# Performance work log

Hardware: AMD Instinct MI355X
Metric: run time of the kernel (lower is better)

## Reference

```python
import jax, jax.numpy as jnp
import numpy as np
from jax import lax

SCORE_TH = 0.05
IOU_TH = 0.5
MAX_DET = 100  # fixed keep budget per class (torch version is variable-length; we pad)
BBOX_STD = jnp.array([0.1, 0.1, 0.2, 0.2], dtype=jnp.float32)


def setup_inputs() -> dict:
    key = jax.random.key(0)
    k1, k2, k3, k4 = jax.random.split(key, 4)
    A, C, H, W = 200000, 80, 768, 768
    # sigmoid-like scores, skewed low so the 0.05 threshold is meaningful
    classification = jax.random.uniform(k1, (A, C), dtype=jnp.float32) ** 4
    regression = jax.random.normal(k2, (A, 4), dtype=jnp.float32)
    ctr = jax.random.uniform(k3, (A, 2), dtype=jnp.float32, minval=0.0, maxval=float(W))
    wh = jax.random.uniform(k4, (A, 2), dtype=jnp.float32, minval=8.0, maxval=128.0)
    anchors = jnp.concatenate([ctr - 0.5 * wh, ctr + 0.5 * wh], axis=-1)  # valid x1y1x2y2
    return {"classification": classification, "regression": regression,
            "anchors": anchors, "img_h": H, "img_w": W}


def _decode_clip(anchors, regression, img_h, img_w):
    # BBoxTransform: RetinaNet delta decode with std [0.1,0.1,0.2,0.2], then ClipBoxes
    wa = anchors[:, 2] - anchors[:, 0]
    ha = anchors[:, 3] - anchors[:, 1]
    cxa = anchors[:, 0] + 0.5 * wa
    cya = anchors[:, 1] + 0.5 * ha
    d = regression * BBOX_STD
    cx = cxa + d[:, 0] * wa
    cy = cya + d[:, 1] * ha
    w = jnp.exp(d[:, 2]) * wa
    h = jnp.exp(d[:, 3]) * ha
    boxes = jnp.stack([cx - 0.5 * w, cy - 0.5 * h, cx + 0.5 * w, cy + 0.5 * h], axis=-1)
    lim = jnp.array([img_w, img_h, img_w, img_h], dtype=boxes.dtype)
    return jnp.clip(boxes, 0.0, lim)


def _nms_one(scores_c, boxes, areas):
    # greedy NMS for one class over all A anchors; fixed MAX_DET iterations
    s0 = jnp.where(scores_c > SCORE_TH, scores_c, -1.0)

    def step(s, _):
        i = jnp.argmax(s)
        valid = s[i] > 0.0
        b = boxes[i]
        xx1 = jnp.maximum(b[0], boxes[:, 0])
        yy1 = jnp.maximum(b[1], boxes[:, 1])
        xx2 = jnp.minimum(b[2], boxes[:, 2])
        yy2 = jnp.minimum(b[3], boxes[:, 3])
        inter = jnp.maximum(xx2 - xx1, 0.0) * jnp.maximum(yy2 - yy1, 0.0)
        iou = inter / (areas[i] + areas - inter)
        supp = (iou > IOU_TH) & valid
        s = jnp.where(supp, -1.0, s).at[i].set(-1.0)
        return s, (i, valid)

    _, (idx, val) = lax.scan(step, s0, None, length=MAX_DET)
    return idx, val  # [MAX_DET] int, [MAX_DET] bool


def _forward(classification, regression, anchors, img_h, img_w):
    boxes = _decode_clip(anchors, regression, img_h, img_w)  # [A,4]
    # NMS index selection is non-differentiable (as in torch); stop_gradient the selection path
    boxes_ng = lax.stop_gradient(boxes)
    scores_ng = lax.stop_gradient(classification)
    areas = (boxes_ng[:, 2] - boxes_ng[:, 0]) * (boxes_ng[:, 3] - boxes_ng[:, 1])
    idx, val = jax.vmap(_nms_one, in_axes=(1, None, None))(scores_ng, boxes_ng, areas)  # [C,M]
    C = classification.shape[1]
    sel_scores = jnp.take_along_axis(classification.T, idx, axis=1) * val          # [C,M]
    sel_boxes = boxes[idx] * val[..., None]                                        # [C,M,4]
    class_ids = jnp.where(val, jnp.arange(C, dtype=jnp.int32)[:, None], -1)        # [C,M]
    # torch returns variable-length concatenations; we return fixed-size padded
    # equivalents (invalid slots: score=0, class=-1, box=0)
    return sel_scores.reshape(-1), class_ids.reshape(-1), sel_boxes.reshape(-1, 4)


def reference(classification, regression, anchors, img_h, img_w):
    return _forward(classification, regression, anchors, img_h, img_w)
```

## Files before the change

### kernel.cpp

```cpp
#include <hip/hip_runtime.h>
#include <float.h>
#include <math.h>

#define SCORE_TH 0.05f
#define IOU_TH   0.5f
#define MAXD     100
#define CAP      512
#define HI_TH    0.996f
#define SWALK    192
#define NWORDS   3
#define CNT_STRIDE 16

__device__ __forceinline__ float4 decode_box(float4 an, float4 r, float W, float H)
{
    float wa = an.z - an.x, ha = an.w - an.y;
    float cxa = an.x + 0.5f * wa, cya = an.y + 0.5f * ha;
    float cx = cxa + r.x * 0.1f * wa;
    float cy = cya + r.y * 0.1f * ha;
    float w  = expf(r.z * 0.2f) * wa;
    float h  = expf(r.w * 0.2f) * ha;
    float x1 = cx - 0.5f * w, y1 = cy - 0.5f * h;
    float x2 = cx + 0.5f * w, y2 = cy + 0.5f * h;
    x1 = fminf(fmaxf(x1, 0.f), W);
    y1 = fminf(fmaxf(y1, 0.f), H);
    x2 = fminf(fmaxf(x2, 0.f), W);
    y2 = fminf(fmaxf(y2, 0.f), H);
    return make_float4(x1, y1, x2, y2);
}

template<int CC>
__global__ __launch_bounds__(256)
void k_compact(const float4* __restrict__ cls4, float2* __restrict__ cand,
               int* __restrict__ cnt, int* __restrict__ loflag,
               int C_rt, int total4)
{
    const int C = CC ? CC : C_rt;
    __shared__ unsigned char lflag[256];
    for (int i = threadIdx.x; i < C; i += blockDim.x) lflag[i] = 0;
    __syncthreads();

    const int gstride = gridDim.x * blockDim.x;
    const int gtid = blockIdx.x * blockDim.x + threadIdx.x;

    for (int j0 = gtid; j0 < total4; j0 += 4 * gstride) {
        int j1 = j0 + gstride, j2 = j0 + 2 * gstride, j3 = j0 + 3 * gstride;
        bool ok1 = j1 < total4, ok2 = j2 < total4, ok3 = j3 < total4;
        float4 v0 = cls4[j0];
        float4 v1 = ok1 ? cls4[j1] : make_float4(0.f, 0.f, 0.f, 0.f);
        float4 v2 = ok2 ? cls4[j2] : make_float4(0.f, 0.f, 0.f, 0.f);
        float4 v3 = ok3 ? cls4[j3] : make_float4(0.f, 0.f, 0.f, 0.f);

        #pragma unroll
        for (int w = 0; w < 4; w++) {
            float4 v = (w == 0) ? v0 : (w == 1) ? v1 : (w == 2) ? v2 : v3;
            if (w == 1 && !ok1) break;
            if (w == 2 && !ok2) break;
            if (w == 3 && !ok3) break;
            unsigned b = (unsigned)(j0 + w * gstride) * 4u;
            int c = (int)(b % (unsigned)C);
            int a = (int)(b / (unsigned)C);
            float s[4] = {v.x, v.y, v.z, v.w};
            #pragma unroll
            for (int j = 0; j < 4; j++) {
                float sc = s[j];
                if (sc > HI_TH) {
                    int pos = atomicAdd(&cnt[c * CNT_STRIDE], 1);
                    if (pos < CAP) cand[(size_t)c * CAP + pos] = make_float2(sc, __int_as_float(a));
                } else if (sc > SCORE_TH) {
                    lflag[c] = 1;
                }
                c++; if (c == C) { c = 0; a++; }
            }
        }
    }
    __syncthreads();
    for (int i = threadIdx.x; i < C; i += blockDim.x)
        if (lflag[i]) loflag[i] = 1;
}

__device__ void fallback_class(const float* __restrict__ cls,
                               const float4* __restrict__ anch, const float4* __restrict__ reg,
                               float W, float H, int A, int C, int c,
                               float* __restrict__ out)
{
    __shared__ float kx1[MAXD], ky1[MAXD], kx2[MAXD], ky2[MAXD], kar[MAXD];
    __shared__ float rs[4]; __shared__ int ra[4];
    __shared__ float cs; __shared__ int caid; __shared__ int have; __shared__ int suppflag;
    int lane = threadIdx.x & 63, wid = threadIdx.x >> 6;
    float s_last = FLT_MAX; int a_last = -1;
    int kept = 0;
    int total = C * MAXD;
    for (long long guard = 0; guard <= (long long)A && kept < MAXD; guard++) {
        float bs = -1.f; int ba = 0x7fffffff;
        for (int a = threadIdx.x; a < A; a += blockDim.x) {
            float s = cls[(size_t)a * C + c];
            if (s <= SCORE_TH) continue;
            if (s > s_last || (s == s_last && a <= a_last)) continue;
            if (s > bs || (s == bs && a < ba)) { bs = s; ba = a; }
        }
        for (int off = 32; off >= 1; off >>= 1) {
            float s2 = __shfl_down(bs, off);
            int a2 = __shfl_down(ba, off);
            if (s2 > bs || (s2 == bs && a2 < ba)) { bs = s2; ba = a2; }
        }
        if (lane == 0) { rs[wid] = bs; ra[wid] = ba; }
        __syncthreads();
        if (threadIdx.x == 0) {
            float fs = rs[0]; int fa = ra[0];
            for (int w = 1; w < 4; w++)
                if (rs[w] > fs || (rs[w] == fs && ra[w] < fa)) { fs = rs[w]; fa = ra[w]; }
            cs = fs; caid = fa; have = (fs > 0.f) ? 1 : 0;
        }
        __syncthreads();
        if (!have) break;
        float s_c = cs; int a_c = caid;
        s_last = s_c; a_last = a_c;
        float4 b = decode_box(anch[a_c], reg[a_c], W, H);
        float ar = (b.z - b.x) * (b.w - b.y);
        if (threadIdx.x == 0) suppflag = 0;
        __syncthreads();
        for (int k = threadIdx.x; k < kept; k += blockDim.x) {
            float xx1 = fmaxf(b.x, kx1[k]);
            float yy1 = fmaxf(b.y, ky1[k]);
            float xx2 = fminf(b.z, kx2[k]);
            float yy2 = fminf(b.w, ky2[k]);
            float inter = fmaxf(xx2 - xx1, 0.f) * fmaxf(yy2 - yy1, 0.f);
            float iou = inter / (ar + kar[k] - inter);
            if (iou > IOU_TH) suppflag = 1;
        }
        __syncthreads();
        if (!suppflag) {
            if (threadIdx.x == 0) {
                kx1[kept] = b.x; ky1[kept] = b.y; kx2[kept] = b.z; ky2[kept] = b.w; kar[kept] = ar;
                int slot = c * MAXD + kept;
                out[slot] = s_c;
                out[total + slot] = (float)c;
                float* ob = out + 2 * (size_t)total + (size_t)slot * 4;
                ob[0] = b.x; ob[1] = b.y; ob[2] = b.z; ob[3] = b.w;
            }
            kept++;
        }
        __syncthreads();
    }
    for (int k = kept + threadIdx.x; k < MAXD; k += blockDim.x) {
        int slot = c * MAXD + k;
        out[slot] = 0.f;
        out[total + slot] = -1.f;
        float* ob = out + 2 * (size_t)total + (size_t)slot * 4;
        ob[0] = 0.f; ob[1] = 0.f; ob[2] = 0.f; ob[3] = 0.f;
    }
}

__global__ __launch_bounds__(256)
void k_nms(const float* __restrict__ cls,
           const float4* __restrict__ anch, const float4* __restrict__ reg,
           const int* __restrict__ ph, const int* __restrict__ pw,
           const float2* __restrict__ cand, const int* __restrict__ cnt,
           const int* __restrict__ loflag,
           float* __restrict__ out, int A, int C)
{
    int c = blockIdx.x;
    __shared__ __align__(16) unsigned long long keys_raw[CAP];
    __shared__ unsigned long long keys[SWALK];
    __shared__ float bx1[SWALK], by1[SWALK], bx2[SWALK], by2[SWALK], sar[SWALK];
    __shared__ __align__(16) unsigned long long m0[SWALK], m1[SWALK], m2[SWALK];
    __shared__ int kidx[MAXD];

    float W = (float)(*pw), H = (float)(*ph);
    int n_raw = cnt[c * CNT_STRIDE];
    if (n_raw > CAP) {
        fallback_class(cls, anch, reg, W, H, A, C, c, out);
        return;
    }
    int n = n_raw;
    int nS = n < SWALK ? n : SWALK;

    for (int i = threadIdx.x; i < n; i += blockDim.x) {
        float2 e = cand[(size_t)c * CAP + i];
        unsigned sbits = __float_as_uint(e.x);
        unsigned aid   = (unsigned)__float_as_int(e.y);
        keys_raw[i] = ((unsigned long long)(~sbits) << 32) | (unsigned long long)aid;
    }
    __syncthreads();

    for (int i = threadIdx.x; i < n; i += blockDim.x) {
        unsigned long long ki = keys_raw[i];
        int r = 0;
        int j = 0;
        for (; j + 2 <= n; j += 2) {
            ulonglong2 kj = *(const ulonglong2*)&keys_raw[j];
            r += (kj.x < ki) + (kj.y < ki);
        }
        if (j < n) r += (keys_raw[j] < ki);
        if (r < SWALK) {
            keys[r] = ki;
            unsigned aid = (unsigned)ki;
            float4 b = decode_box(anch[aid], reg[aid], W, H);
            bx1[r] = b.x; by1[r] = b.y; bx2[r] = b.z; by2[r] = b.w;
            sar[r] = (b.z - b.x) * (b.w - b.y);
        }
    }
    __syncthreads();

    for (int task = threadIdx.x; task < nS * NWORDS; task += blockDim.x) {
        int i = task / NWORDS;
        int w = task - i * NWORDS;
        unsigned long long m = 0ull;
        int j0 = w << 6;
        int jend = j0 + 64 < nS ? j0 + 64 : nS;
        int js = j0 > i + 1 ? j0 : i + 1;
        float ix1 = bx1[i], iy1 = by1[i], ix2 = bx2[i], iy2 = by2[i], ia = sar[i];
        for (int j = js; j < jend; ++j) {
            float xx1 = fmaxf(ix1, bx1[j]);
            float yy1 = fmaxf(iy1, by1[j]);
            float xx2 = fminf(ix2, bx2[j]);
            float yy2 = fminf(iy2, by2[j]);
            float inter = fmaxf(xx2 - xx1, 0.f) * fmaxf(yy2 - yy1, 0.f);
            float iou = inter / (ia + sar[j] - inter);
            if (iou > IOU_TH) m |= 1ull << (j - j0);
        }
        if (w == 0) m0[i] = m; else if (w == 1) m1[i] = m; else m2[i] = m;
    }
    __syncthreads();

    unsigned long long rem0 = 0, rem1 = 0, rem2 = 0;
    int kept = 0;
    ulonglong2 A0 = *(const ulonglong2*)&m0[0], A1 = *(const ulonglong2*)&m0[2];
    ulonglong2 B0 = *(const ulonglong2*)&m1[0], B1 = *(const ulonglong2*)&m1[2];
    ulonglong2 Q0 = *(const ulonglong2*)&m2[0], Q1 = *(const ulonglong2*)&m2[2];
    for (int k0 = 0; k0 < nS && kept < MAXD; k0 += 4) {
        ulonglong2 nA0, nA1, nB0, nB1, nQ0, nQ1;
        int kn = k0 + 4;
        if (kn < nS) {
            nA0 = *(const ulonglong2*)&m0[kn]; nA1 = *(const ulonglong2*)&m0[kn + 2];
            nB0 = *(const ulonglong2*)&m1[kn]; nB1 = *(const ulonglong2*)&m1[kn + 2];
            nQ0 = *(const ulonglong2*)&m2[kn]; nQ1 = *(const ulonglong2*)&m2[kn + 2];
        }
        unsigned long long g = A0.x | A0.y | A1.x | A1.y | B0.x | B0.y | B1.x | B1.y
                             | Q0.x | Q0.y | Q1.x | Q1.y;
        unsigned long long rw4 = ((k0 < 64) ? rem0 : (k0 < 128) ? rem1 : rem2) >> (k0 & 63);
        if (g == 0ull && (rw4 & 0xFull) == 0ull && k0 + 4 <= nS && kept + 4 <= MAXD) {
            if (threadIdx.x == 0) {
                kidx[kept] = k0; kidx[kept + 1] = k0 + 1;
                kidx[kept + 2] = k0 + 2; kidx[kept + 3] = k0 + 3;
            }
            kept += 4;
        } else {
            #pragma unroll
            for (int s = 0; s < 4; ++s) {
                int k = k0 + s;
                if (k < nS && kept < MAXD) {
                    unsigned long long mm0 = (s == 0) ? A0.x : (s == 1) ? A0.y : (s == 2) ? A1.x : A1.y;
                    unsigned long long mm1 = (s == 0) ? B0.x : (s == 1) ? B0.y : (s == 2) ? B1.x : B1.y;
                    unsigned long long mm2 = (s == 0) ? Q0.x : (s == 1) ? Q0.y : (s == 2) ? Q1.x : Q1.y;
                    unsigned long long rw = (k < 64) ? rem0 : (k < 128) ? rem1 : rem2;
                    if (!((rw >> (k & 63)) & 1ull)) {
                        if (threadIdx.x == 0) kidx[kept] = k;
                        ++kept;
                        rem0 |= mm0; rem1 |= mm1; rem2 |= mm2;
                    }
                }
            }
        }
        A0 = nA0; A1 = nA1; B0 = nB0; B1 = nB1; Q0 = nQ0; Q1 = nQ1;
    }
    __syncthreads();

    if (kept < MAXD && (n > nS || loflag[c] != 0)) {
        fallback_class(cls, anch, reg, W, H, A, C, c, out);
        return;
    }

    int total = C * MAXD;
    int base = c * MAXD;
    for (int m = threadIdx.x; m < kept; m += blockDim.x) {
        int k = kidx[m];
        unsigned long long key = keys[k];
        float sc = __uint_as_float(~(unsigned)(key >> 32));
        out[base + m] = sc;
        out[total + base + m] = (float)c;
        float* ob = out + 2 * (size_t)total + (size_t)(base + m) * 4;
        ob[0] = bx1[k]; ob[1] = by1[k]; ob[2] = bx2[k]; ob[3] = by2[k];
    }
    for (int m = kept + threadIdx.x; m < MAXD; m += blockDim.x) {
        out[base + m] = 0.f;
        out[total + base + m] = -1.f;
        float* ob = out + 2 * (size_t)total + (size_t)(base + m) * 4;
        ob[0] = 0.f; ob[1] = 0.f; ob[2] = 0.f; ob[3] = 0.f;
    }
}

extern "C" void kernel_launch(void* const* d_in, const int* in_sizes, int n_in,
                              void* d_out, int out_size, void* d_ws, size_t ws_size,
                              hipStream_t stream)
{
    const float*  cls  = (const float*)d_in[0];
    const float4* reg  = (const float4*)d_in[1];
    const float4* anch = (const float4*)d_in[2];
    const int*    ph   = (const int*)d_in[3];
    const int*    pw   = (const int*)d_in[4];
    int A = in_sizes[1] / 4;
    int C = in_sizes[0] / A;
    float* out = (float*)d_out;

    char* ws = (char*)d_ws;
    float2* cand = (float2*)ws;
    int* ctrl   = (int*)(cand + (size_t)C * CAP);
    int* cnt    = ctrl;
    int* loflag = ctrl + C * CNT_STRIDE;

    hipMemsetAsync(ctrl, 0, (C * CNT_STRIDE + C) * sizeof(int), stream);

    int total4 = (int)((long long)A * C / 4);
    int blocks2 = (total4 + 255) / 256;
    if (blocks2 > 2048) blocks2 = 2048;
    if (C == 80 && (long long)A * C < (1LL << 31))
        k_compact<80><<<blocks2, 256, 0, stream>>>((const float4*)cls, cand, cnt, loflag, C, total4);
    else
        k_compact<0><<<blocks2, 256, 0, stream>>>((const float4*)cls, cand, cnt, loflag, C, total4);

    k_nms<<<C, 256, 0, stream>>>(cls, anch, reg, ph, pw, cand, cnt, loflag, out, A, C);
}
```

Baseline: 136.2 us.

## Decode boxes during compaction and replace serial NMS walk with parallel fixed-point iteration

Box decode and area computation move into the compaction kernel, so each candidate record carries its box and the NMS kernel skips the dependent gather from anchors and regression. The suppression matrix is transposed so each candidate holds a mask of earlier boxes that suppress it. The single-thread greedy walk becomes a block-wide fixed-point iteration: each thread tests whether any currently-kept predecessor suppresses it, and ballots form the new keep mask until it stops changing. Output positions come from popcounts. Costs are a larger candidate record, more shared memory, and an iteration count that can approach the chain length, each round paying two block barriers.

```diff
diff --git a/kernel.cpp b/kernel.cpp
--- a/kernel.cpp
+++ b/kernel.cpp
@@ -28,9 +28,14 @@
     return make_float4(x1, y1, x2, y2);
 }
 
+struct CandRec { float4 a; float4 b; };
+
 template<int CC>
 __global__ __launch_bounds__(256)
-void k_compact(const float4* __restrict__ cls4, float2* __restrict__ cand,
+void k_compact(const float4* __restrict__ cls4,
+               const float4* __restrict__ anch, const float4* __restrict__ reg,
+               const int* __restrict__ ph, const int* __restrict__ pw,
+               CandRec* __restrict__ cand,
                int* __restrict__ cnt, int* __restrict__ loflag,
                int C_rt, int total4)
 {
@@ -39,6 +44,7 @@
     for (int i = threadIdx.x; i < C; i += blockDim.x) lflag[i] = 0;
     __syncthreads();
 
+    float W = (float)(*pw), H = (float)(*ph);
     const int gstride = gridDim.x * blockDim.x;
     const int gtid = blockIdx.x * blockDim.x + threadIdx.x;
 
@@ -65,7 +71,13 @@
                 float sc = s[j];
                 if (sc > HI_TH) {
                     int pos = atomicAdd(&cnt[c * CNT_STRIDE], 1);
-                    if (pos < CAP) cand[(size_t)c * CAP + pos] = make_float2(sc, __int_as_float(a));
+                    if (pos < CAP) {
+                        float4 bx = decode_box(anch[a], reg[a], W, H);
+                        float area = (bx.z - bx.x) * (bx.w - bx.y);
+                        CandRec* r = &cand[(size_t)c * CAP + pos];
+                        r->a = make_float4(sc, __int_as_float(a), bx.x, bx.y);
+                        r->b = make_float4(bx.z, bx.w, area, 0.f);
+                    }
                 } else if (sc > SCORE_TH) {
                     lflag[c] = 1;
                 }
@@ -155,18 +167,23 @@
 void k_nms(const float* __restrict__ cls,
            const float4* __restrict__ anch, const float4* __restrict__ reg,
            const int* __restrict__ ph, const int* __restrict__ pw,
-           const float2* __restrict__ cand, const int* __restrict__ cnt,
+           const CandRec* __restrict__ cand, const int* __restrict__ cnt,
            const int* __restrict__ loflag,
            float* __restrict__ out, int A, int C)
 {
     int c = blockIdx.x;
     __shared__ __align__(16) unsigned long long keys_raw[CAP];
+    __shared__ float4 box_u[CAP];
+    __shared__ float  sar_u[CAP];
     __shared__ unsigned long long keys[SWALK];
-    __shared__ float bx1[SWALK], by1[SWALK], bx2[SWALK], by2[SWALK], sar[SWALK];
-    __shared__ __align__(16) unsigned long long m0[SWALK], m1[SWALK], m2[SWALK];
-    __shared__ int kidx[MAXD];
+    __shared__ float4 box[SWALK];
+    __shared__ float  sar[SWALK];
+    __shared__ unsigned long long t0[SWALK], t1[SWALK], t2[SWALK];
+    __shared__ unsigned long long kw[NWORDS], newkw[NWORDS];
+    __shared__ int changed;
 
     float W = (float)(*pw), H = (float)(*ph);
+    int tid = threadIdx.x;
     int n_raw = cnt[c * CNT_STRIDE];
     if (n_raw > CAP) {
         fallback_class(cls, anch, reg, W, H, A, C, c, out);
@@ -175,15 +192,17 @@
     int n = n_raw;
     int nS = n < SWALK ? n : SWALK;
 
-    for (int i = threadIdx.x; i < n; i += blockDim.x) {
-        float2 e = cand[(size_t)c * CAP + i];
-        unsigned sbits = __float_as_uint(e.x);
-        unsigned aid   = (unsigned)__float_as_int(e.y);
+    for (int i = tid; i < n; i += blockDim.x) {
+        CandRec rec = cand[(size_t)c * CAP + i];
+        unsigned sbits = __float_as_uint(rec.a.x);
+        unsigned aid   = (unsigned)__float_as_int(rec.a.y);
         keys_raw[i] = ((unsigned long long)(~sbits) << 32) | (unsigned long long)aid;
-    }
-    __syncthreads();
-
-    for (int i = threadIdx.x; i < n; i += blockDim.x) {
+        box_u[i] = make_float4(rec.a.z, rec.a.w, rec.b.x, rec.b.y);
+        sar_u[i] = rec.b.z;
+    }
+    __syncthreads();
+
+    for (int i = tid; i < n; i += blockDim.x) {
         unsigned long long ki = keys_raw[i];
         int r = 0;
         int j = 0;
@@ -194,95 +213,91 @@
         if (j < n) r += (keys_raw[j] < ki);
         if (r < SWALK) {
             keys[r] = ki;
-            unsigned aid = (unsigned)ki;
-            float4 b = decode_box(anch[aid], reg[aid], W, H);
-            bx1[r] = b.x; by1[r] = b.y; bx2[r] = b.z; by2[r] = b.w;
-            sar[r] = (b.z - b.x) * (b.w - b.y);
-        }
-    }
-    __syncthreads();
-
-    for (int task = threadIdx.x; task < nS * NWORDS; task += blockDim.x) {
-        int i = task / NWORDS;
-        int w = task - i * NWORDS;
+            box[r] = box_u[i];
+            sar[r] = sar_u[i];
+        }
+    }
+    __syncthreads();
+
+    for (int task = tid; task < nS * NWORDS; task += blockDim.x) {
+        int k = task / NWORDS;
+        int w = task - k * NWORDS;
         unsigned long long m = 0ull;
-        int j0 = w << 6;
-        int jend = j0 + 64 < nS ? j0 + 64 : nS;
-        int js = j0 > i + 1 ? j0 : i + 1;
-        float ix1 = bx1[i], iy1 = by1[i], ix2 = bx2[i], iy2 = by2[i], ia = sar[i];
-        for (int j = js; j < jend; ++j) {
-            float xx1 = fmaxf(ix1, bx1[j]);
-            float yy1 = fmaxf(iy1, by1[j]);
-            float xx2 = fminf(ix2, bx2[j]);
-            float yy2 = fminf(iy2, by2[j]);
-            float inter = fmaxf(xx2 - xx1, 0.f) * fmaxf(yy2 - yy1, 0.f);
-            float iou = inter / (ia + sar[j] - inter);
-            if (iou > IOU_TH) m |= 1ull << (j - j0);
-        }
-        if (w == 0) m0[i] = m; else if (w == 1) m1[i] = m; else m2[i] = m;
-    }
-    __syncthreads();
-
-    unsigned long long rem0 = 0, rem1 = 0, rem2 = 0;
-    int kept = 0;
-    ulonglong2 A0 = *(const ulonglong2*)&m0[0], A1 = *(const ulonglong2*)&m0[2];
-    ulonglong2 B0 = *(const ulonglong2*)&m1[0], B1 = *(const ulonglong2*)&m1[2];
-    ulonglong2 Q0 = *(const ulonglong2*)&m2[0], Q1 = *(const ulonglong2*)&m2[2];
-    for (int k0 = 0; k0 < nS && kept < MAXD; k0 += 4) {
-        ulonglong2 nA0, nA1, nB0, nB1, nQ0, nQ1;
-        int kn = k0 + 4;
-        if (kn < nS) {
-            nA0 = *(const ulonglong2*)&m0[kn]; nA1 = *(const ulonglong2*)&m0[kn + 2];
-            nB0 = *(const ulonglong2*)&m1[kn]; nB1 = *(const ulonglong2*)&m1[kn + 2];
-            nQ0 = *(const ulonglong2*)&m2[kn]; nQ1 = *(const ulonglong2*)&m2[kn + 2];
-        }
-        unsigned long long g = A0.x | A0.y | A1.x | A1.y | B0.x | B0.y | B1.x | B1.y
-                             | Q0.x | Q0.y | Q1.x | Q1.y;
-        unsigned long long rw4 = ((k0 < 64) ? rem0 : (k0 < 128) ? rem1 : rem2) >> (k0 & 63);
-        if (g == 0ull && (rw4 & 0xFull) == 0ull && k0 + 4 <= nS && kept + 4 <= MAXD) {
-            if (threadIdx.x == 0) {
-                kidx[kept] = k0; kidx[kept + 1] = k0 + 1;
-                kidx[kept + 2] = k0 + 2; kidx[kept + 3] = k0 + 3;
+        int i0 = w << 6;
+        int iend = (i0 + 64 < k) ? (i0 + 64) : k;
+        if (i0 < iend) {
+            float4 bk = box[k]; float ak = sar[k];
+            for (int i = i0; i < iend; ++i) {
+                float4 bi = box[i];
+                float xx1 = fmaxf(bk.x, bi.x);
+                float yy1 = fmaxf(bk.y, bi.y);
+                float xx2 = fminf(bk.z, bi.z);
+                float yy2 = fminf(bk.w, bi.w);
+                float inter = fmaxf(xx2 - xx1, 0.f) * fmaxf(yy2 - yy1, 0.f);
+                float iou = inter / (ak + sar[i] - inter);
+                if (iou > IOU_TH) m |= 1ull << (i - i0);
             }
-            kept += 4;
-        } else {
-            #pragma unroll
-            for (int s = 0; s < 4; ++s) {
-                int k = k0 + s;
-                if (k < nS && kept < MAXD) {
-                    unsigned long long mm0 = (s == 0) ? A0.x : (s == 1) ? A0.y : (s == 2) ? A1.x : A1.y;
-                    unsigned long long mm1 = (s == 0) ? B0.x : (s == 1) ? B0.y : (s == 2) ? B1.x : B1.y;
-                    unsigned long long mm2 = (s == 0) ? Q0.x : (s == 1) ? Q0.y : (s == 2) ? Q1.x : Q1.y;
-                    unsigned long long rw = (k < 64) ? rem0 : (k < 128) ? rem1 : rem2;
-                    if (!((rw >> (k & 63)) & 1ull)) {
-                        if (threadIdx.x == 0) kidx[kept] = k;
-                        ++kept;
-                        rem0 |= mm0; rem1 |= mm1; rem2 |= mm2;
-                    }
-                }
-            }
-        }
-        A0 = nA0; A1 = nA1; B0 = nB0; B1 = nB1; Q0 = nQ0; Q1 = nQ1;
-    }
-    __syncthreads();
-
-    if (kept < MAXD && (n > nS || loflag[c] != 0)) {
+        }
+        if (w == 0) t0[k] = m; else if (w == 1) t1[k] = m; else t2[k] = m;
+    }
+    if (tid == 0) {
+        kw[0] = (nS >= 64) ? ~0ull : ((nS <= 0) ? 0ull : ((1ull << nS) - 1));
+        int r1 = nS - 64;
+        kw[1] = (r1 >= 64) ? ~0ull : ((r1 <= 0) ? 0ull : ((1ull << r1) - 1));
+        int r2 = nS - 128;
+        kw[2] = (r2 >= 64) ? ~0ull : ((r2 <= 0) ? 0ull : ((1ull << r2) - 1));
+    }
+    __syncthreads();
+
+    for (int iter = 0; iter <= nS; ++iter) {
+        bool kept_k = false;
+        if (tid < nS) {
+            unsigned long long r = (t0[tid] & kw[0]) | (t1[tid] & kw[1]) | (t2[tid] & kw[2]);
+            kept_k = (r == 0ull);
+        }
+        unsigned long long b = __ballot(kept_k);
+        if ((tid & 63) == 0 && (tid >> 6) < NWORDS) newkw[tid >> 6] = b;
+        __syncthreads();
+        if (tid == 0) {
+            changed = (newkw[0] != kw[0]) || (newkw[1] != kw[1]) || (newkw[2] != kw[2]);
+            kw[0] = newkw[0]; kw[1] = newkw[1]; kw[2] = newkw[2];
+        }
+        __syncthreads();
+        if (!changed) break;
+    }
+
+    unsigned long long k0r = kw[0], k1r = kw[1], k2r = kw[2];
+    int kept_total = __popcll(k0r) + __popcll(k1r) + __popcll(k2r);
+
+    if (kept_total < MAXD && (n > nS || loflag[c] != 0)) {
+        __syncthreads();
         fallback_class(cls, anch, reg, W, H, A, C, c, out);
         return;
     }
 
     int total = C * MAXD;
     int base = c * MAXD;
-    for (int m = threadIdx.x; m < kept; m += blockDim.x) {
-        int k = kidx[m];
-        unsigned long long key = keys[k];
-        float sc = __uint_as_float(~(unsigned)(key >> 32));
-        out[base + m] = sc;
-        out[total + base + m] = (float)c;
-        float* ob = out + 2 * (size_t)total + (size_t)(base + m) * 4;
-        ob[0] = bx1[k]; ob[1] = by1[k]; ob[2] = bx2[k]; ob[3] = by2[k];
-    }
-    for (int m = kept + threadIdx.x; m < MAXD; m += blockDim.x) {
+    if (tid < nS) {
+        int k = tid;
+        unsigned long long myw = (k < 64) ? k0r : (k < 128) ? k1r : k2r;
+        if ((myw >> (k & 63)) & 1ull) {
+            int pos = 0;
+            if (k >= 64)  pos += __popcll(k0r);
+            if (k >= 128) pos += __popcll(k1r);
+            pos += __popcll(myw & ((1ull << (k & 63)) - 1ull));
+            if (pos < MAXD) {
+                unsigned long long key = keys[k];
+                float sc = __uint_as_float(~(unsigned)(key >> 32));
+                out[base + pos] = sc;
+                out[total + base + pos] = (float)c;
+                float4 bb = box[k];
+                float* ob = out + 2 * (size_t)total + (size_t)(base + pos) * 4;
+                ob[0] = bb.x; ob[1] = bb.y; ob[2] = bb.z; ob[3] = bb.w;
+            }
+        }
+    }
+    int keptN = kept_total < MAXD ? kept_total : MAXD;
+    for (int m = keptN + tid; m < MAXD; m += blockDim.x) {
         out[base + m] = 0.f;
         out[total + base + m] = -1.f;
         float* ob = out + 2 * (size_t)total + (size_t)(base + m) * 4;
@@ -304,7 +319,7 @@
     float* out = (float*)d_out;
 
     char* ws = (char*)d_ws;
-    float2* cand = (float2*)ws;
+    CandRec* cand = (CandRec*)ws;
     int* ctrl   = (int*)(cand + (size_t)C * CAP);
     int* cnt    = ctrl;
     int* loflag = ctrl + C * CNT_STRIDE;
@@ -315,9 +330,11 @@
     int blocks2 = (total4 + 255) / 256;
     if (blocks2 > 2048) blocks2 = 2048;
     if (C == 80 && (long long)A * C < (1LL << 31))
-        k_compact<80><<<blocks2, 256, 0, stream>>>((const float4*)cls, cand, cnt, loflag, C, total4);
+        k_compact<80><<<blocks2, 256, 0, stream>>>((const float4*)cls, anch, reg, ph, pw,
+                                                   cand, cnt, loflag, C, total4);
     else
-        k_compact<0><<<blocks2, 256, 0, stream>>>((const float4*)cls, cand, cnt, loflag, C, total4);
+        k_compact<0><<<blocks2, 256, 0, stream>>>((const float4*)cls, anch, reg, ph, pw,
+                                                  cand, cnt, loflag, C, total4);
 
     k_nms<<<C, 256, 0, stream>>>(cls, anch, reg, ph, pw, cand, cnt, loflag, out, A, C);
 }
```

Measured after the change: 128.1 us. -5.9%, faster.
